# Optimization experiments

Hardware: AMD Instinct MI355X
Metric: run time of the kernel (lower is better)

The kernel has to match this reference:

```python
import jax, jax.numpy as jnp
import numpy as np


def setup_inputs() -> dict:
    key = jax.random.key(0)
    k1, k2, k3, k4, k5 = jax.random.split(key, 5)
    B, S, F = 16384, 8192, 512
    inputs = jax.random.normal(k1, (B, F), dtype=jnp.float32)
    support_vectors = jax.random.normal(k2, (S, F), dtype=jnp.float32)
    coefficients = jax.random.uniform(k3, (1, S), dtype=jnp.float32)
    rho = jax.random.uniform(k4, (1,), dtype=jnp.float32)
    # small positive gamma typical of RBF kernels on normalized features
    gamma = jax.random.uniform(k5, (), dtype=jnp.float32) * jnp.float32(0.01)
    return {"inputs": inputs, "support_vectors": support_vectors,
            "coefficients": coefficients, "rho": rho, "gamma": gamma}


def reference(inputs, support_vectors, coefficients, rho, gamma):
    # (same math as the broadcast-subtract-square-sum in the original,
    #  without materializing the [B, S, F] intermediate)
    x_sq = jnp.sum(inputs * inputs, axis=1, keepdims=True)          # [B, 1]
    s_sq = jnp.sum(support_vectors * support_vectors, axis=1)       # [S]
    cross = inputs @ support_vectors.T                              # [B, S]
    d2 = x_sq + s_sq[None, :] - 2.0 * cross                         # [B, S]
    k = jnp.exp(-gamma * d2)                                        # [B, S]
    score = jnp.sum(k * coefficients, axis=1)                       # [B]
    return score - rho                                              # rho broadcasts [1] -> [B]
```

## Files before the change

kernel.cpp:

```cpp
#include <hip/hip_runtime.h>
#include <stdint.h>
#include <stddef.h>

#define BROWS  16384
#define SROWS  8192
#define FDIM   512
#define NCHUNK 4
#define SCHUNK (SROWS / NCHUNK)
#define BN     32
#define NTILES (SCHUNK / BN)
#define BM     256
#define KSTEPS (FDIM / 16)

#define LOG2E 1.44269504088896340736f

typedef __bf16 bf16x8 __attribute__((ext_vector_type(8)));
typedef float  f32x16 __attribute__((ext_vector_type(16)));

__device__ inline void gload16(const void* g, void* l) {
  __builtin_amdgcn_global_load_lds(
      (const __attribute__((address_space(1))) void*)g,
      (__attribute__((address_space(3))) void*)l, 16, 0, 0);
}

__global__ __launch_bounds__(256) void prep_s_kernel(
    const float* __restrict__ S, const float* __restrict__ coeff,
    const float* __restrict__ gamma, __bf16* __restrict__ Sb,
    float* __restrict__ lc2)
{
  const int lane = threadIdx.x & 63;
  const int wid  = threadIdx.x >> 6;
  const int row  = (blockIdx.x << 2) + wid;
  const float* src = S + ((size_t)row << 9) + (lane << 3);
  float4 a = ((const float4*)src)[0];
  float4 b = ((const float4*)src)[1];
  float sq = a.x*a.x + a.y*a.y + a.z*a.z + a.w*a.w +
             b.x*b.x + b.y*b.y + b.z*b.z + b.w*b.w;
  bf16x8 v;
  v[0]=(__bf16)a.x; v[1]=(__bf16)a.y; v[2]=(__bf16)a.z; v[3]=(__bf16)a.w;
  v[4]=(__bf16)b.x; v[5]=(__bf16)b.y; v[6]=(__bf16)b.z; v[7]=(__bf16)b.w;
  *(bf16x8*)(Sb + ((size_t)row << 9) + (lane << 3)) = v;
  #pragma unroll
  for (int m = 1; m < 64; m <<= 1) sq += __shfl_xor(sq, m, 64);
  if (lane == 0) {
    float g = gamma[0];
    lc2[row] = log2f(coeff[row]) - g * LOG2E * sq;
  }
}

__global__ __launch_bounds__(512, 2) void ocsvm_main_kernel(
    const float* __restrict__ X, const __bf16* __restrict__ Sb,
    const float* __restrict__ lc2, const float* __restrict__ gamma,
    float* __restrict__ partials)
{
  __shared__ char lds[98304];
  const int tid  = threadIdx.x;
  const int wid  = tid >> 6;
  const int lane = tid & 63;
  const int col  = lane & 31;
  const int half = lane >> 5;

  const int bx    = blockIdx.x;
  const int xcd   = bx & 7;
  const int grp   = bx >> 3;
  const int chunk = xcd >> 1;
  const int mtile = (grp << 1) + (xcd & 1);
  const int m0    = mtile * BM;
  const int chunk0 = chunk * SCHUNK;

  const float gam = gamma[0];
  const float K2  = 2.0f * gam * LOG2E;

#define STAGE(bufsel, tile)                                                   \
  {                                                                           \
    _Pragma("unroll")                                                         \
    for (int r = 0; r < 4; ++r) {                                             \
      const int t_all = (r << 9) + tid;                                       \
      const int cs = t_all & 31;                                              \
      const int kb = t_all >> 5;                                              \
      const char* src = (const char*)Sb +                                     \
          (((size_t)(chunk0 + ((tile) << 5) + cs)) << 10) + (kb << 4);        \
      char* dst = &lds[(bufsel) * 32768 + (((r << 9) + (wid << 6)) << 4)];    \
      gload16(src, dst);                                                      \
    }                                                                         \
  }

  STAGE(0, 0);

  const int arow = m0 + (wid << 5) + col;
  const float* xp = X + ((size_t)arow << 9) + (half << 3);
  bf16x8 afrag[KSTEPS];
  float sq = 0.0f;
  #pragma unroll
  for (int ks = 0; ks < KSTEPS; ++ks) {
    float4 a = *(const float4*)(xp + (ks << 4));
    float4 b = *(const float4*)(xp + (ks << 4) + 4);
    sq += a.x*a.x + a.y*a.y + a.z*a.z + a.w*a.w +
          b.x*b.x + b.y*b.y + b.z*b.z + b.w*b.w;
    bf16x8 v;
    v[0]=(__bf16)a.x; v[1]=(__bf16)a.y; v[2]=(__bf16)a.z; v[3]=(__bf16)a.w;
    v[4]=(__bf16)b.x; v[5]=(__bf16)b.y; v[6]=(__bf16)b.z; v[7]=(__bf16)b.w;
    afrag[ks] = v;
  }
  sq += __shfl_xor(sq, 32, 64);
  const float e_x = __builtin_amdgcn_exp2f(-gam * LOG2E * sq);

  float scoreAcc[16];
  #pragma unroll
  for (int i = 0; i < 16; ++i) scoreAcc[i] = 0.0f;

  const char* bread0 = &lds[(half << 9) + (col << 4)];
  const float* lc2p = lc2 + chunk0 + col;

  int cur = 0;
  for (int t = 0; t < NTILES; ++t) {
    int nxt = cur + 1; if (nxt == 3) nxt = 0;
    if (t + 1 < NTILES) {
      STAGE(nxt, t + 1);
      asm volatile("s_waitcnt vmcnt(4)" ::: "memory");
    } else {
      asm volatile("s_waitcnt vmcnt(0)" ::: "memory");
    }
    __builtin_amdgcn_s_barrier();
    asm volatile("" ::: "memory");

    const char* bb = bread0 + cur * 32768;
    f32x16 acc0 = {};
    f32x16 acc1 = {};
    #pragma unroll
    for (int ks = 0; ks < KSTEPS; ks += 2) {
      bf16x8 b0 = *(const bf16x8*)(bb + (ks << 10));
      bf16x8 b1 = *(const bf16x8*)(bb + ((ks + 1) << 10));
      acc0 = __builtin_amdgcn_mfma_f32_32x32x16_bf16(afrag[ks],     b0, acc0, 0, 0, 0);
      acc1 = __builtin_amdgcn_mfma_f32_32x32x16_bf16(afrag[ks + 1], b1, acc1, 0, 0, 0);
    }

    const float lc2v = lc2p[t << 5];
    #pragma unroll
    for (int r2 = 0; r2 < 16; ++r2) {
      scoreAcc[r2] += __builtin_amdgcn_exp2f(
          __builtin_fmaf(K2, acc0[r2], __builtin_fmaf(K2, acc1[r2], lc2v)));
    }
    cur = nxt;
  }

  #pragma unroll
  for (int r2 = 0; r2 < 16; ++r2) {
    float v = scoreAcc[r2];
    v += __shfl_xor(v, 1, 64);
    v += __shfl_xor(v, 2, 64);
    v += __shfl_xor(v, 4, 64);
    v += __shfl_xor(v, 8, 64);
    v += __shfl_xor(v, 16, 64);
    const int rloc = (r2 & 3) + ((r2 >> 2) << 3) + (half << 2);
    const float exr = __shfl(e_x, rloc, 64);
    if (col == 0)
      partials[chunk * BROWS + m0 + (wid << 5) + rloc] = exr * v;
  }
#undef STAGE
}

__global__ __launch_bounds__(256) void reduce_kernel(
    const float* __restrict__ partials, const float* __restrict__ rho,
    float* __restrict__ out)
{
  const int i = blockIdx.x * 256 + threadIdx.x;
  float s = partials[i] + partials[BROWS + i] +
            partials[2 * BROWS + i] + partials[3 * BROWS + i];
  out[i] = s - rho[0];
}

extern "C" void kernel_launch(void* const* d_in, const int* in_sizes, int n_in,
                              void* d_out, int out_size, void* d_ws, size_t ws_size,
                              hipStream_t stream) {
  const float* X     = (const float*)d_in[0];
  const float* S     = (const float*)d_in[1];
  const float* coeff = (const float*)d_in[2];
  const float* rho   = (const float*)d_in[3];
  const float* gamma = (const float*)d_in[4];
  float* out = (float*)d_out;

  char* ws = (char*)d_ws;
  __bf16* Sb    = (__bf16*)ws;
  float*  lc2   = (float*)(ws + (size_t)SROWS * FDIM * 2);
  float*  parts = (float*)(ws + (size_t)SROWS * FDIM * 2 + SROWS * 4);

  prep_s_kernel<<<SROWS / 4, 256, 0, stream>>>(S, coeff, gamma, Sb, lc2);
  ocsvm_main_kernel<<<NCHUNK * 64, 512, 0, stream>>>(X, Sb, lc2, gamma, parts);
  reduce_kernel<<<BROWS / 256, 256, 0, stream>>>(parts, rho, out);
}
```

Baseline: 151.4 us.

## Retile main GEMM to 256x256x64 LDS tiles with 16x16 MFMA and X prep kernel

Adds a separate kernel that converts X to bf16 and precomputes exp(-gamma*||x||^2). The main kernel now stages both A and B tiles (256x256, K chunks of 64) through double-buffered, XOR-swizzled LDS and computes 8x4 tiles of 16x16x32 MFMAs per wave, instead of holding X fragments in registers and streaming 32-wide S tiles. This is meant to raise arithmetic intensity and MFMA utilisation per LDS load. In exchange it adds an extra kernel pass over X, a 128KB LDS footprint, and four times as many partial sums for the reduce kernel, which now sums 16 partials per row.

```diff
diff --git a/kernel.cpp b/kernel.cpp
--- a/kernel.cpp
+++ b/kernel.cpp
@@ -7,15 +7,17 @@
 #define FDIM   512
 #define NCHUNK 4
 #define SCHUNK (SROWS / NCHUNK)
-#define BN     32
-#define NTILES (SCHUNK / BN)
 #define BM     256
-#define KSTEPS (FDIM / 16)
+#define BN     256
+#define BK     64
+#define NSTILE (SCHUNK / BN)
+#define NKC    (FDIM / BK)
+#define NC     (NSTILE * NKC)
 
 #define LOG2E 1.44269504088896340736f
 
 typedef __bf16 bf16x8 __attribute__((ext_vector_type(8)));
-typedef float  f32x16 __attribute__((ext_vector_type(16)));
+typedef float  f32x4  __attribute__((ext_vector_type(4)));
 
 __device__ inline void gload16(const void* g, void* l) {
   __builtin_amdgcn_global_load_lds(
@@ -42,121 +44,143 @@
   *(bf16x8*)(Sb + ((size_t)row << 9) + (lane << 3)) = v;
   #pragma unroll
   for (int m = 1; m < 64; m <<= 1) sq += __shfl_xor(sq, m, 64);
-  if (lane == 0) {
-    float g = gamma[0];
-    lc2[row] = log2f(coeff[row]) - g * LOG2E * sq;
+  if (lane == 0) lc2[row] = log2f(coeff[row]) - gamma[0] * LOG2E * sq;
+}
+
+__global__ __launch_bounds__(256) void prep_x_kernel(
+    const float* __restrict__ X, const float* __restrict__ gamma,
+    __bf16* __restrict__ Xb, float* __restrict__ ex)
+{
+  const int lane = threadIdx.x & 63;
+  const int wid  = threadIdx.x >> 6;
+  const int row  = (blockIdx.x << 2) + wid;
+  const float* src = X + ((size_t)row << 9) + (lane << 3);
+  float4 a = ((const float4*)src)[0];
+  float4 b = ((const float4*)src)[1];
+  float sq = a.x*a.x + a.y*a.y + a.z*a.z + a.w*a.w +
+             b.x*b.x + b.y*b.y + b.z*b.z + b.w*b.w;
+  bf16x8 v;
+  v[0]=(__bf16)a.x; v[1]=(__bf16)a.y; v[2]=(__bf16)a.z; v[3]=(__bf16)a.w;
+  v[4]=(__bf16)b.x; v[5]=(__bf16)b.y; v[6]=(__bf16)b.z; v[7]=(__bf16)b.w;
+  *(bf16x8*)(Xb + ((size_t)row << 9) + (lane << 3)) = v;
+  #pragma unroll
+  for (int m = 1; m < 64; m <<= 1) sq += __shfl_xor(sq, m, 64);
+  if (lane == 0) ex[row] = exp2f(-gamma[0] * LOG2E * sq);
+}
+
+__global__ __launch_bounds__(512, 2) void ocsvm_main_kernel(
+    const __bf16* __restrict__ Xb, const __bf16* __restrict__ Sb,
+    const float* __restrict__ lc2, const float* __restrict__ ex,
+    const float* __restrict__ gamma, float* __restrict__ partials)
+{
+  __shared__ char lds[131072];
+  const int tid  = threadIdx.x;
+  const int lane = tid & 63;
+  const int wid  = tid >> 6;
+  const int wm   = wid >> 2;
+  const int wn   = wid & 3;
+  const int lr   = lane & 15;
+  const int hi   = lane >> 4;
+
+  const int bx      = blockIdx.x;
+  const int xcd     = bx & 7;
+  const int grp     = bx >> 3;
+  const int chunkid = xcd >> 1;
+  const int mtile   = (grp << 1) + (xcd & 1);
+  const int m0      = mtile * BM;
+  const int chunk0  = chunkid * SCHUNK;
+
+  const float K2 = 2.0f * gamma[0] * LOG2E;
+
+  const char* xb = (const char*)Xb;
+  const char* sb = (const char*)Sb;
+  const int r0     = tid >> 3;
+  const int srcoff = ((tid & 7) << 4) ^ ((r0 & 7) << 4);
+
+#define STAGE(bufsel, c)                                                      \
+  { const int st_ = (c) >> 3, kc_ = (c) & 7;                                  \
+    const char* asrc_ = xb + (((size_t)(m0 + r0)) << 10) + (kc_ << 7) + srcoff; \
+    const char* bsrc_ = sb + (((size_t)(chunk0 + (st_ << 8) + r0)) << 10)     \
+                           + (kc_ << 7) + srcoff;                             \
+    char* ad_ = &lds[(bufsel) * 65536 + (tid << 4)];                          \
+    _Pragma("unroll")                                                         \
+    for (int j = 0; j < 4; ++j) {                                             \
+      gload16(asrc_ + j * 65536, ad_ + j * 8192);                             \
+      gload16(bsrc_ + j * 65536, ad_ + 32768 + j * 8192);                     \
+    } }
+
+  const int sw0 = (hi << 4) ^ ((lr & 7) << 4);
+  const int sw1 = sw0 ^ 64;
+
+  float score[8][4];
+  #pragma unroll
+  for (int mi = 0; mi < 8; ++mi)
+    #pragma unroll
+    for (int j = 0; j < 4; ++j) score[mi][j] = 0.0f;
+
+  STAGE(0, 0);
+
+  int c = 0;
+  for (int st = 0; st < NSTILE; ++st) {
+    f32x4 acc[8][4];
+    #pragma unroll
+    for (int mi = 0; mi < 8; ++mi)
+      #pragma unroll
+      for (int ni = 0; ni < 4; ++ni) acc[mi][ni] = (f32x4){0.f, 0.f, 0.f, 0.f};
+
+    for (int kc = 0; kc < NKC; ++kc, ++c) {
+      asm volatile("s_waitcnt vmcnt(0)" ::: "memory");
+      __builtin_amdgcn_s_barrier();
+      asm volatile("" ::: "memory");
+      if (c + 1 < NC) STAGE((c + 1) & 1, c + 1);
+
+      const char* bA = &lds[(c & 1) * 65536 + wm * 16384 + lr * 128];
+      const char* bB = &lds[(c & 1) * 65536 + 32768 + (wn << 13) + lr * 128];
+
+      #pragma unroll
+      for (int ks = 0; ks < 2; ++ks) {
+        const int swk = ks ? sw1 : sw0;
+        bf16x8 bfr[4], af[8];
+        #pragma unroll
+        for (int ni = 0; ni < 4; ++ni)
+          bfr[ni] = *(const bf16x8*)(bB + swk + ni * 2048);
+        #pragma unroll
+        for (int mi = 0; mi < 8; ++mi)
+          af[mi] = *(const bf16x8*)(bA + swk + mi * 2048);
+        #pragma unroll
+        for (int mi = 0; mi < 8; ++mi)
+          #pragma unroll
+          for (int ni = 0; ni < 4; ++ni)
+            acc[mi][ni] = __builtin_amdgcn_mfma_f32_16x16x32_bf16(
+                af[mi], bfr[ni], acc[mi][ni], 0, 0, 0);
+      }
+    }
+
+    const float* lc = lc2 + chunk0 + (st << 8) + (wn << 6) + lr;
+    const float l0 = lc[0], l1 = lc[16], l2 = lc[32], l3 = lc[48];
+    #pragma unroll
+    for (int mi = 0; mi < 8; ++mi)
+      #pragma unroll
+      for (int j = 0; j < 4; ++j)
+        score[mi][j] += __builtin_amdgcn_exp2f(__builtin_fmaf(K2, acc[mi][0][j], l0))
+                      + __builtin_amdgcn_exp2f(__builtin_fmaf(K2, acc[mi][1][j], l1))
+                      + __builtin_amdgcn_exp2f(__builtin_fmaf(K2, acc[mi][2][j], l2))
+                      + __builtin_amdgcn_exp2f(__builtin_fmaf(K2, acc[mi][3][j], l3));
   }
-}
-
-__global__ __launch_bounds__(512, 2) void ocsvm_main_kernel(
-    const float* __restrict__ X, const __bf16* __restrict__ Sb,
-    const float* __restrict__ lc2, const float* __restrict__ gamma,
-    float* __restrict__ partials)
-{
-  __shared__ char lds[98304];
-  const int tid  = threadIdx.x;
-  const int wid  = tid >> 6;
-  const int lane = tid & 63;
-  const int col  = lane & 31;
-  const int half = lane >> 5;
-
-  const int bx    = blockIdx.x;
-  const int xcd   = bx & 7;
-  const int grp   = bx >> 3;
-  const int chunk = xcd >> 1;
-  const int mtile = (grp << 1) + (xcd & 1);
-  const int m0    = mtile * BM;
-  const int chunk0 = chunk * SCHUNK;
-
-  const float gam = gamma[0];
-  const float K2  = 2.0f * gam * LOG2E;
-
-#define STAGE(bufsel, tile)                                                   \
-  {                                                                           \
-    _Pragma("unroll")                                                         \
-    for (int r = 0; r < 4; ++r) {                                             \
-      const int t_all = (r << 9) + tid;                                       \
-      const int cs = t_all & 31;                                              \
-      const int kb = t_all >> 5;                                              \
-      const char* src = (const char*)Sb +                                     \
-          (((size_t)(chunk0 + ((tile) << 5) + cs)) << 10) + (kb << 4);        \
-      char* dst = &lds[(bufsel) * 32768 + (((r << 9) + (wid << 6)) << 4)];    \
-      gload16(src, dst);                                                      \
-    }                                                                         \
-  }
-
-  STAGE(0, 0);
-
-  const int arow = m0 + (wid << 5) + col;
-  const float* xp = X + ((size_t)arow << 9) + (half << 3);
-  bf16x8 afrag[KSTEPS];
-  float sq = 0.0f;
-  #pragma unroll
-  for (int ks = 0; ks < KSTEPS; ++ks) {
-    float4 a = *(const float4*)(xp + (ks << 4));
-    float4 b = *(const float4*)(xp + (ks << 4) + 4);
-    sq += a.x*a.x + a.y*a.y + a.z*a.z + a.w*a.w +
-          b.x*b.x + b.y*b.y + b.z*b.z + b.w*b.w;
-    bf16x8 v;
-    v[0]=(__bf16)a.x; v[1]=(__bf16)a.y; v[2]=(__bf16)a.z; v[3]=(__bf16)a.w;
-    v[4]=(__bf16)b.x; v[5]=(__bf16)b.y; v[6]=(__bf16)b.z; v[7]=(__bf16)b.w;
-    afrag[ks] = v;
-  }
-  sq += __shfl_xor(sq, 32, 64);
-  const float e_x = __builtin_amdgcn_exp2f(-gam * LOG2E * sq);
-
-  float scoreAcc[16];
-  #pragma unroll
-  for (int i = 0; i < 16; ++i) scoreAcc[i] = 0.0f;
-
-  const char* bread0 = &lds[(half << 9) + (col << 4)];
-  const float* lc2p = lc2 + chunk0 + col;
-
-  int cur = 0;
-  for (int t = 0; t < NTILES; ++t) {
-    int nxt = cur + 1; if (nxt == 3) nxt = 0;
-    if (t + 1 < NTILES) {
-      STAGE(nxt, t + 1);
-      asm volatile("s_waitcnt vmcnt(4)" ::: "memory");
-    } else {
-      asm volatile("s_waitcnt vmcnt(0)" ::: "memory");
+
+  #pragma unroll
+  for (int mi = 0; mi < 8; ++mi)
+    #pragma unroll
+    for (int j = 0; j < 4; ++j) {
+      float v = score[mi][j];
+      v += __shfl_xor(v, 1, 64);
+      v += __shfl_xor(v, 2, 64);
+      v += __shfl_xor(v, 4, 64);
+      v += __shfl_xor(v, 8, 64);
+      const int row = m0 + (wm << 7) + (mi << 4) + (hi << 2) + j;
+      if (lr == 0)
+        partials[(size_t)((chunkid << 2) + wn) * BROWS + row] = ex[row] * v;
     }
-    __builtin_amdgcn_s_barrier();
-    asm volatile("" ::: "memory");
-
-    const char* bb = bread0 + cur * 32768;
-    f32x16 acc0 = {};
-    f32x16 acc1 = {};
-    #pragma unroll
-    for (int ks = 0; ks < KSTEPS; ks += 2) {
-      bf16x8 b0 = *(const bf16x8*)(bb + (ks << 10));
-      bf16x8 b1 = *(const bf16x8*)(bb + ((ks + 1) << 10));
-      acc0 = __builtin_amdgcn_mfma_f32_32x32x16_bf16(afrag[ks],     b0, acc0, 0, 0, 0);
-      acc1 = __builtin_amdgcn_mfma_f32_32x32x16_bf16(afrag[ks + 1], b1, acc1, 0, 0, 0);
-    }
-
-    const float lc2v = lc2p[t << 5];
-    #pragma unroll
-    for (int r2 = 0; r2 < 16; ++r2) {
-      scoreAcc[r2] += __builtin_amdgcn_exp2f(
-          __builtin_fmaf(K2, acc0[r2], __builtin_fmaf(K2, acc1[r2], lc2v)));
-    }
-    cur = nxt;
-  }
-
-  #pragma unroll
-  for (int r2 = 0; r2 < 16; ++r2) {
-    float v = scoreAcc[r2];
-    v += __shfl_xor(v, 1, 64);
-    v += __shfl_xor(v, 2, 64);
-    v += __shfl_xor(v, 4, 64);
-    v += __shfl_xor(v, 8, 64);
-    v += __shfl_xor(v, 16, 64);
-    const int rloc = (r2 & 3) + ((r2 >> 2) << 3) + (half << 2);
-    const float exr = __shfl(e_x, rloc, 64);
-    if (col == 0)
-      partials[chunk * BROWS + m0 + (wid << 5) + rloc] = exr * v;
-  }
 #undef STAGE
 }
 
@@ -165,8 +189,9 @@
     float* __restrict__ out)
 {
   const int i = blockIdx.x * 256 + threadIdx.x;
-  float s = partials[i] + partials[BROWS + i] +
-            partials[2 * BROWS + i] + partials[3 * BROWS + i];
+  float s = 0.0f;
+  #pragma unroll
+  for (int k = 0; k < 16; ++k) s += partials[(size_t)k * BROWS + i];
   out[i] = s - rho[0];
 }
 
@@ -182,10 +207,13 @@
 
   char* ws = (char*)d_ws;
   __bf16* Sb    = (__bf16*)ws;
-  float*  lc2   = (float*)(ws + (size_t)SROWS * FDIM * 2);
-  float*  parts = (float*)(ws + (size_t)SROWS * FDIM * 2 + SROWS * 4);
+  __bf16* Xbuf  = (__bf16*)(ws + ((size_t)SROWS * FDIM * 2));
+  float*  lc2   = (float*)(ws + ((size_t)SROWS * FDIM * 2) + ((size_t)BROWS * FDIM * 2));
+  float*  ex    = lc2 + SROWS;
+  float*  parts = ex + BROWS;
 
   prep_s_kernel<<<SROWS / 4, 256, 0, stream>>>(S, coeff, gamma, Sb, lc2);
-  ocsvm_main_kernel<<<NCHUNK * 64, 512, 0, stream>>>(X, Sb, lc2, gamma, parts);
+  prep_x_kernel<<<BROWS / 4, 256, 0, stream>>>(X, gamma, Xbuf, ex);
+  ocsvm_main_kernel<<<NCHUNK * 64, 512, 0, stream>>>(Xbuf, Sb, lc2, ex, gamma, parts);
   reduce_kernel<<<BROWS / 256, 256, 0, stream>>>(parts, rho, out);
 }
```

Measured after the change: 248.3 us. +64.0%, slower.
